# Kernel optimization log

Measured on AMD Instinct MI355X. Metric: run time of the kernel, lower is better.

Reference implementation:

```python
import jax, jax.numpy as jnp
import numpy as np

B, C = 2048, 5000          # batchSize, classNum
LLR_REL = 0.9              # keep-rate; k = ceil(B*C*(1-llr_rel))
K = int(np.ceil(B * C * (1.0 - LLR_REL)))
MARGIN = 0.0


def _bce_with_logits(x, t):
    # elementwise BCEWithLogitsLoss (reduce=False): max(x,0) - x*t + log1p(exp(-|x|))
    return jnp.maximum(x, 0.0) - x * t + jnp.log1p(jnp.exp(-jnp.abs(x)))


def setup_inputs() -> dict:
    key = jax.random.key(0)
    k1, k2 = jax.random.split(key)
    inp = jax.random.normal(k1, (B, C), dtype=jnp.float32)
    # target in {-1, 0, +1}: -1 negative, 0 unobserved/ignored, +1 positive
    tgt = (jax.random.randint(k2, (B, C), 0, 3) - 1).astype(jnp.float32)
    return {"input": inp, "target": tgt, "k": K}


def reference(input, target, k):
    input = input.astype(jnp.float32)
    target = target.astype(jnp.float32)
    positive_mask = (target > MARGIN).astype(jnp.float32)
    negative_mask = (target < -MARGIN).astype(jnp.float32)
    positive_loss = _bce_with_logits(input, target)
    negative_loss = _bce_with_logits(-input, -target)
    unobserved_loss = negative_mask * negative_loss
    if k != 0:
        # k-th largest value of the flattened unobserved loss is the threshold
        topk_vals = jax.lax.top_k(unobserved_loss.reshape(-1), k)[0]
        topk_lossvalue = topk_vals[-1]
        loss_mask = (unobserved_loss < topk_lossvalue).astype(jnp.float32)
        negative_mask = negative_mask * loss_mask
    loss = positive_mask * positive_loss + negative_mask * negative_loss
    return loss
```

## Files before the change

kernel.cpp:

```cpp
#include <hip/hip_runtime.h>
#include <cstdint>


struct SelState {
    uint32_t prefix;
    uint32_t k_rem;
    uint32_t u_kth;
    float    thr_nl;
    uint32_t done;
};

#define GUARD 256u

__device__ __forceinline__ uint32_t xform(uint32_t b) {
    return ((int32_t)b < 0) ? ~b : (b | 0x80000000u);
}
__device__ __forceinline__ float unxform(uint32_t u) {
    uint32_t b = (u & 0x80000000u) ? (u ^ 0x80000000u) : ~u;
    return __uint_as_float(b);
}
__device__ __forceinline__ float neg_loss_precise(float x, float t) {
#pragma clang fp contract(off)
    return (fmaxf(-x, 0.0f) - x * t) + log1pf(expf(-fabsf(x)));
}

__device__ __forceinline__ void hist_quad(uint32_t* my, float4 xv, float4 tv) {
    uint32_t u0 = (tv.x < 0.0f) ? xform(__float_as_uint(xv.x)) : 0u;
    uint32_t u1 = (tv.y < 0.0f) ? xform(__float_as_uint(xv.y)) : 0u;
    uint32_t u2 = (tv.z < 0.0f) ? xform(__float_as_uint(xv.z)) : 0u;
    uint32_t u3 = (tv.w < 0.0f) ? xform(__float_as_uint(xv.w)) : 0u;
    if (u0) atomicAdd(&my[u0 >> 21], 1u);
    if (u1) atomicAdd(&my[u1 >> 21], 1u);
    if (u2) atomicAdd(&my[u2 >> 21], 1u);
    if (u3) atomicAdd(&my[u3 >> 21], 1u);
}

__global__ __launch_bounds__(256) void k1_hist(
        const float* __restrict__ x, const float* __restrict__ t,
        uint32_t* __restrict__ hist, int n) {
    __shared__ uint32_t lh[2 * 2049];
    for (int i = threadIdx.x; i < 2 * 2049; i += 256) lh[i] = 0;
    __syncthreads();
    uint32_t* my = &lh[(threadIdx.x & 1) * 2049];

    const float4* x4 = (const float4*)x;
    const float4* t4 = (const float4*)t;
    const int n4 = n >> 2;
    const int S = gridDim.x * 256;
    int i = blockIdx.x * 256 + threadIdx.x;
    for (; i + 3 * S < n4; i += 4 * S) {
        float4 xa = x4[i], xb = x4[i + S], xc = x4[i + 2 * S], xd = x4[i + 3 * S];
        float4 ta = t4[i], tb = t4[i + S], tc = t4[i + 2 * S], td = t4[i + 3 * S];
        hist_quad(my, xa, ta);
        hist_quad(my, xb, tb);
        hist_quad(my, xc, tc);
        hist_quad(my, xd, td);
    }
    for (; i < n4; i += S) {
        float4 xa = x4[i], ta = t4[i];
        hist_quad(my, xa, ta);
    }
    if (blockIdx.x == 0) {
        for (int j = (n4 << 2) + threadIdx.x; j < n; j += 256) {
            uint32_t u = (t[j] < 0.0f) ? xform(__float_as_uint(x[j])) : 0u;
            if (u) atomicAdd(&my[u >> 21], 1u);
        }
    }
    __syncthreads();
    for (int b = threadIdx.x; b < 2048; b += 256) {
        uint32_t c = lh[b] + lh[2049 + b];
        if (c) atomicAdd(&hist[b], c);
    }
}

__global__ __launch_bounds__(256) void scan1(
        const uint32_t* __restrict__ hist, SelState* __restrict__ st,
        const int* __restrict__ kptr) {
    __shared__ uint32_t part[256];
    const int tid = threadIdx.x;
    uint32_t cnt[8];
    uint32_t lsum = 0;
#pragma unroll
    for (int j = 0; j < 8; ++j) { cnt[j] = hist[tid * 8 + j]; lsum += cnt[j]; }
    part[tid] = lsum;
    __syncthreads();
    for (int off = 1; off < 256; off <<= 1) {
        uint32_t add = (tid + off < 256) ? part[tid + off] : 0u;
        __syncthreads();
        part[tid] += add;
        __syncthreads();
    }
    const uint32_t total = part[0];
    int kk = *kptr;
    uint32_t k = (kk > 0) ? (uint32_t)kk : 0u;
    if (k == 0u) {
        if (tid == 0) { st->u_kth = 0xFFFFFFFFu; st->thr_nl = __int_as_float(0x7F800000); st->done = 1u; }
        return;
    }
    if (k > total) {
        if (tid == 0) { st->u_kth = 0u; st->thr_nl = 0.0f; st->done = 1u; }
        return;
    }
    uint32_t A = (tid < 255) ? part[tid + 1] : 0u;
#pragma unroll
    for (int j = 7; j >= 0; --j) {
        uint32_t c = cnt[j];
        if (A < k && k <= A + c) {
            st->prefix = (uint32_t)(tid * 8 + j);
            st->k_rem = k - A;
        }
        A += c;
    }
}

__device__ __forceinline__ void cnt_quad(uint32_t* __restrict__ h21, uint32_t pref,
                                         float4 xv, float4 tv) {
    uint32_t u0 = (tv.x < 0.0f) ? xform(__float_as_uint(xv.x)) : 0u;
    uint32_t u1 = (tv.y < 0.0f) ? xform(__float_as_uint(xv.y)) : 0u;
    uint32_t u2 = (tv.z < 0.0f) ? xform(__float_as_uint(xv.z)) : 0u;
    uint32_t u3 = (tv.w < 0.0f) ? xform(__float_as_uint(xv.w)) : 0u;
    if (u0 && (u0 >> 21) == pref) atomicAdd(&h21[u0 & 0x1FFFFFu], 1u);
    if (u1 && (u1 >> 21) == pref) atomicAdd(&h21[u1 & 0x1FFFFFu], 1u);
    if (u2 && (u2 >> 21) == pref) atomicAdd(&h21[u2 & 0x1FFFFFu], 1u);
    if (u3 && (u3 >> 21) == pref) atomicAdd(&h21[u3 & 0x1FFFFFu], 1u);
}

__global__ __launch_bounds__(256) void k2_hist21(
        const float* __restrict__ x, const float* __restrict__ t,
        uint32_t* __restrict__ h21, const SelState* __restrict__ st, int n) {
    __shared__ uint32_t s_pref, s_done;
    if (threadIdx.x == 0) { s_pref = st->prefix; s_done = st->done; }
    __syncthreads();
    if (s_done) return;
    const uint32_t pref = s_pref;

    const float4* x4 = (const float4*)x;
    const float4* t4 = (const float4*)t;
    const int n4 = n >> 2;
    const int S = gridDim.x * 256;
    int i = blockIdx.x * 256 + threadIdx.x;
    for (; i + 3 * S < n4; i += 4 * S) {
        float4 xa = x4[i], xb = x4[i + S], xc = x4[i + 2 * S], xd = x4[i + 3 * S];
        float4 ta = t4[i], tb = t4[i + S], tc = t4[i + 2 * S], td = t4[i + 3 * S];
        cnt_quad(h21, pref, xa, ta);
        cnt_quad(h21, pref, xb, tb);
        cnt_quad(h21, pref, xc, tc);
        cnt_quad(h21, pref, xd, td);
    }
    for (; i < n4; i += S) {
        float4 xa = x4[i], ta = t4[i];
        cnt_quad(h21, pref, xa, ta);
    }
    if (blockIdx.x == 0) {
        for (int j = (n4 << 2) + threadIdx.x; j < n; j += 256) {
            uint32_t u = (t[j] < 0.0f) ? xform(__float_as_uint(x[j])) : 0u;
            if (u && (u >> 21) == pref) atomicAdd(&h21[u & 0x1FFFFFu], 1u);
        }
    }
}

__global__ __launch_bounds__(256) void scan2a(
        const uint32_t* __restrict__ h21, uint32_t* __restrict__ csums,
        const SelState* __restrict__ st) {
    __shared__ uint32_t red[256];
    __shared__ uint32_t s_done;
    if (threadIdx.x == 0) s_done = st->done;
    __syncthreads();
    if (s_done) return;
    const uint4* b4 = (const uint4*)(h21 + (size_t)blockIdx.x * 2048);
    uint32_t s = 0;
    for (int j = threadIdx.x; j < 512; j += 256) {
        uint4 v = b4[j];
        s += v.x + v.y + v.z + v.w;
    }
    red[threadIdx.x] = s;
    __syncthreads();
    for (int off = 128; off > 0; off >>= 1) {
        if (threadIdx.x < off) red[threadIdx.x] += red[threadIdx.x + off];
        __syncthreads();
    }
    if (threadIdx.x == 0) csums[blockIdx.x] = red[0];
}

__global__ __launch_bounds__(256) void scan2b(
        const uint32_t* __restrict__ h21, const uint32_t* __restrict__ csums,
        SelState* __restrict__ st) {
    __shared__ uint32_t part[256];
    __shared__ uint32_t sel[2];
    __shared__ SelState sst;
    const int tid = threadIdx.x;
    if (tid == 0) sst = *st;
    __syncthreads();
    if (sst.done) return;
    const uint32_t k = sst.k_rem;

    uint32_t c4[4];
    uint32_t lsum = 0;
#pragma unroll
    for (int j = 0; j < 4; ++j) { c4[j] = csums[tid * 4 + j]; lsum += c4[j]; }
    part[tid] = lsum;
    __syncthreads();
    for (int off = 1; off < 256; off <<= 1) {
        uint32_t add = (tid + off < 256) ? part[tid + off] : 0u;
        __syncthreads();
        part[tid] += add;
        __syncthreads();
    }
    uint32_t A = (tid < 255) ? part[tid + 1] : 0u;
#pragma unroll
    for (int j = 3; j >= 0; --j) {
        uint32_t c = c4[j];
        if (A < k && k <= A + c) { sel[0] = (uint32_t)(tid * 4 + j); sel[1] = k - A; }
        A += c;
    }
    __syncthreads();
    const uint32_t chunk = sel[0];
    const uint32_t k2 = sel[1];
    __syncthreads();

    const uint32_t* base = h21 + (size_t)chunk * 2048;
    uint32_t b8[8];
    lsum = 0;
#pragma unroll
    for (int j = 0; j < 8; ++j) { b8[j] = base[tid * 8 + j]; lsum += b8[j]; }
    part[tid] = lsum;
    __syncthreads();
    for (int off = 1; off < 256; off <<= 1) {
        uint32_t add = (tid + off < 256) ? part[tid + off] : 0u;
        __syncthreads();
        part[tid] += add;
        __syncthreads();
    }
    A = (tid < 255) ? part[tid + 1] : 0u;
#pragma unroll
    for (int j = 7; j >= 0; --j) {
        uint32_t c = b8[j];
        if (A < k2 && k2 <= A + c) {
            uint32_t u = (sst.prefix << 21) | (chunk * 2048u + (uint32_t)(tid * 8 + j));
            st->u_kth = u;
            st->thr_nl = neg_loss_precise(unxform(u), -1.0f);
            st->done = 1u;
        }
        A += c;
    }
}

__device__ __forceinline__ float fin1(float xx, float tt, uint32_t ukth, float thr) {
    float lp = __logf(1.0f + __expf(-fabsf(xx)));
    float v = 0.0f;
    if (tt > 0.0f) {
        v = fmaxf(xx, 0.0f) - xx * tt + lp;
    } else if (tt < 0.0f) {
        uint32_t u = xform(__float_as_uint(xx));
        bool keep = u < ukth;
        if (keep && (ukth - u) < GUARD)
            keep = neg_loss_precise(xx, tt) < thr;
        if (keep) v = fmaxf(-xx, 0.0f) - xx * tt + lp;
    }
    return v;
}

__device__ __forceinline__ float4 fin_quad(float4 xv, float4 tv, uint32_t ukth, float thr) {
    float4 r;
    r.x = fin1(xv.x, tv.x, ukth, thr);
    r.y = fin1(xv.y, tv.y, ukth, thr);
    r.z = fin1(xv.z, tv.z, ukth, thr);
    r.w = fin1(xv.w, tv.w, ukth, thr);
    return r;
}

__global__ __launch_bounds__(256) void k_final(
        const float* __restrict__ x, const float* __restrict__ t,
        const SelState* __restrict__ st, float* __restrict__ out, int n) {
    const uint32_t ukth = st->u_kth;
    const float thr = st->thr_nl;
    const float4* x4 = (const float4*)x;
    const float4* t4 = (const float4*)t;
    float4* o4 = (float4*)out;
    const int n4 = n >> 2;
    const int S = gridDim.x * 256;
    int i = blockIdx.x * 256 + threadIdx.x;
    for (; i + 3 * S < n4; i += 4 * S) {
        float4 xa = x4[i], xb = x4[i + S], xc = x4[i + 2 * S], xd = x4[i + 3 * S];
        float4 ta = t4[i], tb = t4[i + S], tc = t4[i + 2 * S], td = t4[i + 3 * S];
        o4[i]         = fin_quad(xa, ta, ukth, thr);
        o4[i + S]     = fin_quad(xb, tb, ukth, thr);
        o4[i + 2 * S] = fin_quad(xc, tc, ukth, thr);
        o4[i + 3 * S] = fin_quad(xd, td, ukth, thr);
    }
    for (; i < n4; i += S) {
        float4 xa = x4[i], ta = t4[i];
        o4[i] = fin_quad(xa, ta, ukth, thr);
    }
    if (blockIdx.x == 0) {
        for (int j = (n4 << 2) + threadIdx.x; j < n; j += 256) {
            out[j] = fin1(x[j], t[j], ukth, thr);
        }
    }
}

extern "C" void kernel_launch(void* const* d_in, const int* in_sizes, int n_in,
                              void* d_out, int out_size, void* d_ws, size_t ws_size,
                              hipStream_t stream) {
    const float* x = (const float*)d_in[0];
    const float* t = (const float*)d_in[1];
    const int* kptr = (const int*)d_in[2];
    float* out = (float*)d_out;
    const int n = in_sizes[0];
    if (n <= 0) return;

    char* ws = (char*)d_ws;
    uint32_t* hist1 = (uint32_t*)(ws + 0);
    uint32_t* csums = (uint32_t*)(ws + 8192);
    SelState* st    = (SelState*)(ws + 12288);
    uint32_t* h21   = (uint32_t*)(ws + 16384);

    hipMemsetAsync(d_ws, 0, 16384 + (size_t)(1u << 21) * 4u, stream);

    const int n4 = n >> 2;
    int work = (n4 + 255) / 256;
    if (work < 1) work = 1;
    int grid = work < 1024 ? work : 1024;

    k1_hist  <<<grid, 256, 0, stream>>>(x, t, hist1, n);
    scan1    <<<1, 256, 0, stream>>>(hist1, st, kptr);
    k2_hist21<<<grid, 256, 0, stream>>>(x, t, h21, st, n);
    scan2a   <<<1024, 256, 0, stream>>>(h21, csums, st);
    scan2b   <<<1, 256, 0, stream>>>(h21, csums, st);
    k_final  <<<grid, 256, 0, stream>>>(x, t, st, out, n);
}
```

Before: 177.1 us.

## Compact negative candidates in first pass and refine radix select on compacted list

The first histogram pass now also stream-compacts the transformed keys of negative-target elements into per-wave segments and stores a packed 2-bit class map for each float4 of targets. The second and third radix refinement passes read only the compacted candidates instead of re-reading both full input arrays, and the 8 MB second-level histogram memset is replaced by two small histograms (10-bit and 11-bit). The final pass reads the byte class map instead of the float target array. This cuts global memory traffic and the large memset, at the cost of one extra small kernel and extra writes of candidates and cmap in the first pass.

```diff
diff --git a/kernel.cpp b/kernel.cpp
--- a/kernel.cpp
+++ b/kernel.cpp
@@ -1,10 +1,13 @@
 #include <hip/hip_runtime.h>
 #include <cstdint>
+#include <cstddef>
 
 
 struct SelState {
-    uint32_t prefix;
-    uint32_t k_rem;
+    uint32_t prefix1;
+    uint32_t k1rem;
+    uint32_t prefix2;
+    uint32_t k2rem;
     uint32_t u_kth;
     float    thr_nl;
     uint32_t done;
@@ -24,22 +27,41 @@
     return (fmaxf(-x, 0.0f) - x * t) + log1pf(expf(-fabsf(x)));
 }
 
-__device__ __forceinline__ void hist_quad(uint32_t* my, float4 xv, float4 tv) {
-    uint32_t u0 = (tv.x < 0.0f) ? xform(__float_as_uint(xv.x)) : 0u;
-    uint32_t u1 = (tv.y < 0.0f) ? xform(__float_as_uint(xv.y)) : 0u;
-    uint32_t u2 = (tv.z < 0.0f) ? xform(__float_as_uint(xv.z)) : 0u;
-    uint32_t u3 = (tv.w < 0.0f) ? xform(__float_as_uint(xv.w)) : 0u;
+__device__ __forceinline__ void wscan(uint32_t m, int lane, uint32_t& excl, uint32_t& tot) {
+    uint32_t inc = m;
+#pragma unroll
+    for (int d = 1; d < 64; d <<= 1) {
+        uint32_t v = __shfl_up(inc, (unsigned)d, 64);
+        if (lane >= d) inc += v;
+    }
+    excl = inc - m;
+    tot = __shfl(inc, 63, 64);
+}
+
+__device__ __forceinline__ uint32_t quad_u_cls(uint32_t* my, float4 xv, float4 tv,
+        uint32_t& u0, uint32_t& u1, uint32_t& u2, uint32_t& u3) {
+    u0 = (tv.x < 0.0f) ? xform(__float_as_uint(xv.x)) : 0u;
+    u1 = (tv.y < 0.0f) ? xform(__float_as_uint(xv.y)) : 0u;
+    u2 = (tv.z < 0.0f) ? xform(__float_as_uint(xv.z)) : 0u;
+    u3 = (tv.w < 0.0f) ? xform(__float_as_uint(xv.w)) : 0u;
+    uint32_t cls = ((tv.x > 0.0f) ? 1u : ((tv.x < 0.0f) ? 2u : 0u))
+                 | (((tv.y > 0.0f) ? 1u : ((tv.y < 0.0f) ? 2u : 0u)) << 2)
+                 | (((tv.z > 0.0f) ? 1u : ((tv.z < 0.0f) ? 2u : 0u)) << 4)
+                 | (((tv.w > 0.0f) ? 1u : ((tv.w < 0.0f) ? 2u : 0u)) << 6);
     if (u0) atomicAdd(&my[u0 >> 21], 1u);
     if (u1) atomicAdd(&my[u1 >> 21], 1u);
     if (u2) atomicAdd(&my[u2 >> 21], 1u);
     if (u3) atomicAdd(&my[u3 >> 21], 1u);
+    return cls;
 }
 
 __global__ __launch_bounds__(256) void k1_hist(
         const float* __restrict__ x, const float* __restrict__ t,
-        uint32_t* __restrict__ hist, int n) {
+        uint32_t* __restrict__ hist1, uint32_t* __restrict__ cand1,
+        uint32_t* __restrict__ wvcnt, uint8_t* __restrict__ cmap,
+        int n, int segw) {
     __shared__ uint32_t lh[2 * 2049];
-    for (int i = threadIdx.x; i < 2 * 2049; i += 256) lh[i] = 0;
+    for (int j = threadIdx.x; j < 2 * 2049; j += 256) lh[j] = 0;
     __syncthreads();
     uint32_t* my = &lh[(threadIdx.x & 1) * 2049];
 
@@ -47,41 +69,108 @@
     const float4* t4 = (const float4*)t;
     const int n4 = n >> 2;
     const int S = gridDim.x * 256;
+    const int lane = threadIdx.x & 63;
+    const int wid  = threadIdx.x >> 6;
+    uint32_t* wseg = cand1 + (size_t)(blockIdx.x * 4 + wid) * (size_t)segw;
+    uint32_t wcur = 0;
+
+    int M4 = 0;
+    {
+        long rem = (long)n4 - 1 - (long)(blockIdx.x * 256 + 255);
+        if (rem >= 0) {
+            long T = rem / S;
+            if (T >= 3) M4 = (int)((T - 3) / 4 + 1);
+        }
+    }
     int i = blockIdx.x * 256 + threadIdx.x;
-    for (; i + 3 * S < n4; i += 4 * S) {
+
+    for (int b = 0; b < M4; ++b, i += 4 * S) {
         float4 xa = x4[i], xb = x4[i + S], xc = x4[i + 2 * S], xd = x4[i + 3 * S];
         float4 ta = t4[i], tb = t4[i + S], tc = t4[i + 2 * S], td = t4[i + 3 * S];
-        hist_quad(my, xa, ta);
-        hist_quad(my, xb, tb);
-        hist_quad(my, xc, tc);
-        hist_quad(my, xd, td);
-    }
-    for (; i < n4; i += S) {
-        float4 xa = x4[i], ta = t4[i];
-        hist_quad(my, xa, ta);
-    }
+        uint32_t u0, u1, u2, u3, u4_, u5, u6, u7, u8, u9, uA, uB, uC, uD, uE, uF;
+        uint32_t ca = quad_u_cls(my, xa, ta, u0, u1, u2, u3);
+        uint32_t cb = quad_u_cls(my, xb, tb, u4_, u5, u6, u7);
+        uint32_t cc = quad_u_cls(my, xc, tc, u8, u9, uA, uB);
+        uint32_t cd = quad_u_cls(my, xd, td, uC, uD, uE, uF);
+        cmap[i]         = (uint8_t)ca;
+        cmap[i + S]     = (uint8_t)cb;
+        cmap[i + 2 * S] = (uint8_t)cc;
+        cmap[i + 3 * S] = (uint8_t)cd;
+        uint32_t m = (u0 != 0) + (u1 != 0) + (u2 != 0) + (u3 != 0)
+                   + (u4_ != 0) + (u5 != 0) + (u6 != 0) + (u7 != 0)
+                   + (u8 != 0) + (u9 != 0) + (uA != 0) + (uB != 0)
+                   + (uC != 0) + (uD != 0) + (uE != 0) + (uF != 0);
+        uint32_t excl, tot;
+        wscan(m, lane, excl, tot);
+        uint32_t p = wcur + excl;
+        if (u0)  wseg[p++] = u0;
+        if (u1)  wseg[p++] = u1;
+        if (u2)  wseg[p++] = u2;
+        if (u3)  wseg[p++] = u3;
+        if (u4_) wseg[p++] = u4_;
+        if (u5)  wseg[p++] = u5;
+        if (u6)  wseg[p++] = u6;
+        if (u7)  wseg[p++] = u7;
+        if (u8)  wseg[p++] = u8;
+        if (u9)  wseg[p++] = u9;
+        if (uA)  wseg[p++] = uA;
+        if (uB)  wseg[p++] = uB;
+        if (uC)  wseg[p++] = uC;
+        if (uD)  wseg[p++] = uD;
+        if (uE)  wseg[p++] = uE;
+        if (uF)  wseg[p++] = uF;
+        wcur += tot;
+    }
+
+    for (; __any(i < n4); i += S) {
+        const bool act = i < n4;
+        float4 xa = act ? x4[i] : make_float4(0.f, 0.f, 0.f, 0.f);
+        float4 ta = act ? t4[i] : make_float4(0.f, 0.f, 0.f, 0.f);
+        uint32_t u0, u1, u2, u3;
+        uint32_t ca = quad_u_cls(my, xa, ta, u0, u1, u2, u3);
+        if (act) cmap[i] = (uint8_t)ca;
+        uint32_t m = (u0 != 0) + (u1 != 0) + (u2 != 0) + (u3 != 0);
+        uint32_t excl, tot;
+        wscan(m, lane, excl, tot);
+        uint32_t p = wcur + excl;
+        if (u0) wseg[p++] = u0;
+        if (u1) wseg[p++] = u1;
+        if (u2) wseg[p++] = u2;
+        if (u3) wseg[p++] = u3;
+        wcur += tot;
+    }
+
     if (blockIdx.x == 0) {
-        for (int j = (n4 << 2) + threadIdx.x; j < n; j += 256) {
-            uint32_t u = (t[j] < 0.0f) ? xform(__float_as_uint(x[j])) : 0u;
-            if (u) atomicAdd(&my[u >> 21], 1u);
-        }
-    }
-    __syncthreads();
-    for (int b = threadIdx.x; b < 2048; b += 256) {
-        uint32_t c = lh[b] + lh[2049 + b];
-        if (c) atomicAdd(&hist[b], c);
-    }
-}
-
-__global__ __launch_bounds__(256) void scan1(
-        const uint32_t* __restrict__ hist, SelState* __restrict__ st,
+        int j = (n4 << 2) + threadIdx.x;
+        const bool act = j < n;
+        float xx = act ? x[j] : 0.0f;
+        float tt = act ? t[j] : 0.0f;
+        uint32_t u0 = (tt < 0.0f) ? xform(__float_as_uint(xx)) : 0u;
+        if (u0) atomicAdd(&my[u0 >> 21], 1u);
+        uint32_t excl, tot;
+        wscan(u0 != 0 ? 1u : 0u, lane, excl, tot);
+        if (u0) wseg[wcur + excl] = u0;
+        wcur += tot;
+    }
+
+    if (lane == 0) wvcnt[blockIdx.x * 4 + wid] = wcur;
+
+    __syncthreads();
+    for (int b2 = threadIdx.x; b2 < 2048; b2 += 256) {
+        uint32_t c = lh[b2] + lh[2049 + b2];
+        if (c) atomicAdd(&hist1[b2], c);
+    }
+}
+
+__global__ __launch_bounds__(256) void s1_scan(
+        const uint32_t* __restrict__ hist1, SelState* __restrict__ st,
         const int* __restrict__ kptr) {
     __shared__ uint32_t part[256];
     const int tid = threadIdx.x;
     uint32_t cnt[8];
     uint32_t lsum = 0;
 #pragma unroll
-    for (int j = 0; j < 8; ++j) { cnt[j] = hist[tid * 8 + j]; lsum += cnt[j]; }
+    for (int j = 0; j < 8; ++j) { cnt[j] = hist1[tid * 8 + j]; lsum += cnt[j]; }
     part[tid] = lsum;
     __syncthreads();
     for (int off = 1; off < 256; off <<= 1) {
@@ -106,98 +195,50 @@
     for (int j = 7; j >= 0; --j) {
         uint32_t c = cnt[j];
         if (A < k && k <= A + c) {
-            st->prefix = (uint32_t)(tid * 8 + j);
-            st->k_rem = k - A;
+            st->prefix1 = (uint32_t)(tid * 8 + j);
+            st->k1rem = k - A;
         }
         A += c;
     }
 }
 
-__device__ __forceinline__ void cnt_quad(uint32_t* __restrict__ h21, uint32_t pref,
-                                         float4 xv, float4 tv) {
-    uint32_t u0 = (tv.x < 0.0f) ? xform(__float_as_uint(xv.x)) : 0u;
-    uint32_t u1 = (tv.y < 0.0f) ? xform(__float_as_uint(xv.y)) : 0u;
-    uint32_t u2 = (tv.z < 0.0f) ? xform(__float_as_uint(xv.z)) : 0u;
-    uint32_t u3 = (tv.w < 0.0f) ? xform(__float_as_uint(xv.w)) : 0u;
-    if (u0 && (u0 >> 21) == pref) atomicAdd(&h21[u0 & 0x1FFFFFu], 1u);
-    if (u1 && (u1 >> 21) == pref) atomicAdd(&h21[u1 & 0x1FFFFFu], 1u);
-    if (u2 && (u2 >> 21) == pref) atomicAdd(&h21[u2 & 0x1FFFFFu], 1u);
-    if (u3 && (u3 >> 21) == pref) atomicAdd(&h21[u3 & 0x1FFFFFu], 1u);
-}
-
-__global__ __launch_bounds__(256) void k2_hist21(
-        const float* __restrict__ x, const float* __restrict__ t,
-        uint32_t* __restrict__ h21, const SelState* __restrict__ st, int n) {
+__global__ __launch_bounds__(256) void k2_hist2(
+        const uint32_t* __restrict__ cand1, const uint32_t* __restrict__ wvcnt,
+        uint32_t* __restrict__ hist2, const SelState* __restrict__ st,
+        int nseg, int segw) {
     __shared__ uint32_t s_pref, s_done;
-    if (threadIdx.x == 0) { s_pref = st->prefix; s_done = st->done; }
+    if (threadIdx.x == 0) { s_pref = st->prefix1; s_done = st->done; }
     __syncthreads();
     if (s_done) return;
     const uint32_t pref = s_pref;
-
-    const float4* x4 = (const float4*)x;
-    const float4* t4 = (const float4*)t;
-    const int n4 = n >> 2;
-    const int S = gridDim.x * 256;
-    int i = blockIdx.x * 256 + threadIdx.x;
-    for (; i + 3 * S < n4; i += 4 * S) {
-        float4 xa = x4[i], xb = x4[i + S], xc = x4[i + 2 * S], xd = x4[i + 3 * S];
-        float4 ta = t4[i], tb = t4[i + S], tc = t4[i + 2 * S], td = t4[i + 3 * S];
-        cnt_quad(h21, pref, xa, ta);
-        cnt_quad(h21, pref, xb, tb);
-        cnt_quad(h21, pref, xc, tc);
-        cnt_quad(h21, pref, xd, td);
-    }
-    for (; i < n4; i += S) {
-        float4 xa = x4[i], ta = t4[i];
-        cnt_quad(h21, pref, xa, ta);
-    }
-    if (blockIdx.x == 0) {
-        for (int j = (n4 << 2) + threadIdx.x; j < n; j += 256) {
-            uint32_t u = (t[j] < 0.0f) ? xform(__float_as_uint(x[j])) : 0u;
-            if (u && (u >> 21) == pref) atomicAdd(&h21[u & 0x1FFFFFu], 1u);
-        }
-    }
-}
-
-__global__ __launch_bounds__(256) void scan2a(
-        const uint32_t* __restrict__ h21, uint32_t* __restrict__ csums,
-        const SelState* __restrict__ st) {
-    __shared__ uint32_t red[256];
-    __shared__ uint32_t s_done;
-    if (threadIdx.x == 0) s_done = st->done;
-    __syncthreads();
-    if (s_done) return;
-    const uint4* b4 = (const uint4*)(h21 + (size_t)blockIdx.x * 2048);
-    uint32_t s = 0;
-    for (int j = threadIdx.x; j < 512; j += 256) {
-        uint4 v = b4[j];
-        s += v.x + v.y + v.z + v.w;
-    }
-    red[threadIdx.x] = s;
-    __syncthreads();
-    for (int off = 128; off > 0; off >>= 1) {
-        if (threadIdx.x < off) red[threadIdx.x] += red[threadIdx.x + off];
-        __syncthreads();
-    }
-    if (threadIdx.x == 0) csums[blockIdx.x] = red[0];
-}
-
-__global__ __launch_bounds__(256) void scan2b(
-        const uint32_t* __restrict__ h21, const uint32_t* __restrict__ csums,
-        SelState* __restrict__ st) {
+    for (int s = blockIdx.x; s < nseg; s += gridDim.x) {
+        const uint32_t cnt = wvcnt[s];
+        const uint32_t* base = cand1 + (size_t)s * (size_t)segw;
+        const uint4* b4 = (const uint4*)base;
+        const uint32_t c4 = cnt >> 2;
+        for (uint32_t j = threadIdx.x; j < c4; j += 256) {
+            uint4 v = b4[j];
+            if ((v.x >> 21) == pref) atomicAdd(&hist2[(v.x >> 11) & 1023u], 1u);
+            if ((v.y >> 21) == pref) atomicAdd(&hist2[(v.y >> 11) & 1023u], 1u);
+            if ((v.z >> 21) == pref) atomicAdd(&hist2[(v.z >> 11) & 1023u], 1u);
+            if ((v.w >> 21) == pref) atomicAdd(&hist2[(v.w >> 11) & 1023u], 1u);
+        }
+        if (threadIdx.x < (cnt & 3u)) {
+            uint32_t u = base[(c4 << 2) + threadIdx.x];
+            if ((u >> 21) == pref) atomicAdd(&hist2[(u >> 11) & 1023u], 1u);
+        }
+    }
+}
+
+__global__ __launch_bounds__(256) void s2_scan(
+        const uint32_t* __restrict__ hist2, SelState* __restrict__ st) {
+    if (st->done) return;
     __shared__ uint32_t part[256];
-    __shared__ uint32_t sel[2];
-    __shared__ SelState sst;
     const int tid = threadIdx.x;
-    if (tid == 0) sst = *st;
-    __syncthreads();
-    if (sst.done) return;
-    const uint32_t k = sst.k_rem;
-
-    uint32_t c4[4];
+    uint32_t cnt[4];
     uint32_t lsum = 0;
 #pragma unroll
-    for (int j = 0; j < 4; ++j) { c4[j] = csums[tid * 4 + j]; lsum += c4[j]; }
+    for (int j = 0; j < 4; ++j) { cnt[j] = hist2[tid * 4 + j]; lsum += cnt[j]; }
     part[tid] = lsum;
     __syncthreads();
     for (int off = 1; off < 256; off <<= 1) {
@@ -206,23 +247,59 @@
         part[tid] += add;
         __syncthreads();
     }
+    const uint32_t k = st->k1rem;
     uint32_t A = (tid < 255) ? part[tid + 1] : 0u;
 #pragma unroll
     for (int j = 3; j >= 0; --j) {
-        uint32_t c = c4[j];
-        if (A < k && k <= A + c) { sel[0] = (uint32_t)(tid * 4 + j); sel[1] = k - A; }
+        uint32_t c = cnt[j];
+        if (A < k && k <= A + c) {
+            st->prefix2 = (uint32_t)(tid * 4 + j);
+            st->k2rem = k - A;
+        }
         A += c;
     }
-    __syncthreads();
-    const uint32_t chunk = sel[0];
-    const uint32_t k2 = sel[1];
-    __syncthreads();
-
-    const uint32_t* base = h21 + (size_t)chunk * 2048;
-    uint32_t b8[8];
-    lsum = 0;
-#pragma unroll
-    for (int j = 0; j < 8; ++j) { b8[j] = base[tid * 8 + j]; lsum += b8[j]; }
+}
+
+__global__ __launch_bounds__(256) void k3_hist3(
+        const uint32_t* __restrict__ cand1, const uint32_t* __restrict__ wvcnt,
+        uint32_t* __restrict__ hist3, const SelState* __restrict__ st,
+        int nseg, int segw) {
+    __shared__ uint32_t s_pref21, s_done;
+    if (threadIdx.x == 0) {
+        s_pref21 = (st->prefix1 << 10) | st->prefix2;
+        s_done = st->done;
+    }
+    __syncthreads();
+    if (s_done) return;
+    const uint32_t pref21 = s_pref21;
+    for (int s = blockIdx.x; s < nseg; s += gridDim.x) {
+        const uint32_t cnt = wvcnt[s];
+        const uint32_t* base = cand1 + (size_t)s * (size_t)segw;
+        const uint4* b4 = (const uint4*)base;
+        const uint32_t c4 = cnt >> 2;
+        for (uint32_t j = threadIdx.x; j < c4; j += 256) {
+            uint4 v = b4[j];
+            if ((v.x >> 11) == pref21) atomicAdd(&hist3[v.x & 0x7FFu], 1u);
+            if ((v.y >> 11) == pref21) atomicAdd(&hist3[v.y & 0x7FFu], 1u);
+            if ((v.z >> 11) == pref21) atomicAdd(&hist3[v.z & 0x7FFu], 1u);
+            if ((v.w >> 11) == pref21) atomicAdd(&hist3[v.w & 0x7FFu], 1u);
+        }
+        if (threadIdx.x < (cnt & 3u)) {
+            uint32_t u = base[(c4 << 2) + threadIdx.x];
+            if ((u >> 11) == pref21) atomicAdd(&hist3[u & 0x7FFu], 1u);
+        }
+    }
+}
+
+__global__ __launch_bounds__(256) void s3_scan(
+        const uint32_t* __restrict__ hist3, SelState* __restrict__ st) {
+    if (st->done) return;
+    __shared__ uint32_t part[256];
+    const int tid = threadIdx.x;
+    uint32_t cnt[8];
+    uint32_t lsum = 0;
+#pragma unroll
+    for (int j = 0; j < 8; ++j) { cnt[j] = hist3[tid * 8 + j]; lsum += cnt[j]; }
     part[tid] = lsum;
     __syncthreads();
     for (int off = 1; off < 256; off <<= 1) {
@@ -231,12 +308,13 @@
         part[tid] += add;
         __syncthreads();
     }
-    A = (tid < 255) ? part[tid + 1] : 0u;
+    const uint32_t k = st->k2rem;
+    uint32_t A = (tid < 255) ? part[tid + 1] : 0u;
 #pragma unroll
     for (int j = 7; j >= 0; --j) {
-        uint32_t c = b8[j];
-        if (A < k2 && k2 <= A + c) {
-            uint32_t u = (sst.prefix << 21) | (chunk * 2048u + (uint32_t)(tid * 8 + j));
+        uint32_t c = cnt[j];
+        if (A < k && k <= A + c) {
+            uint32_t u = (st->prefix1 << 21) | (st->prefix2 << 11) | (uint32_t)(tid * 8 + j);
             st->u_kth = u;
             st->thr_nl = neg_loss_precise(unxform(u), -1.0f);
             st->done = 1u;
@@ -245,7 +323,31 @@
     }
 }
 
-__device__ __forceinline__ float fin1(float xx, float tt, uint32_t ukth, float thr) {
+__device__ __forceinline__ float fin1c(float xx, uint32_t cls, uint32_t ukth, float thr) {
+    float lp = __logf(1.0f + __expf(-fabsf(xx)));
+    float v = 0.0f;
+    if (cls == 1u) {
+        v = (fmaxf(xx, 0.0f) - xx) + lp;
+    } else if (cls == 2u) {
+        uint32_t u = xform(__float_as_uint(xx));
+        bool keep = u < ukth;
+        if (keep && (ukth - u) < GUARD)
+            keep = neg_loss_precise(xx, -1.0f) < thr;
+        if (keep) v = (fmaxf(-xx, 0.0f) + xx) + lp;
+    }
+    return v;
+}
+
+__device__ __forceinline__ float4 fin_quadc(float4 xv, uint32_t cb, uint32_t ukth, float thr) {
+    float4 r;
+    r.x = fin1c(xv.x, cb & 3u, ukth, thr);
+    r.y = fin1c(xv.y, (cb >> 2) & 3u, ukth, thr);
+    r.z = fin1c(xv.z, (cb >> 4) & 3u, ukth, thr);
+    r.w = fin1c(xv.w, (cb >> 6) & 3u, ukth, thr);
+    return r;
+}
+
+__device__ __forceinline__ float fin1t(float xx, float tt, uint32_t ukth, float thr) {
     float lp = __logf(1.0f + __expf(-fabsf(xx)));
     float v = 0.0f;
     if (tt > 0.0f) {
@@ -260,41 +362,33 @@
     return v;
 }
 
-__device__ __forceinline__ float4 fin_quad(float4 xv, float4 tv, uint32_t ukth, float thr) {
-    float4 r;
-    r.x = fin1(xv.x, tv.x, ukth, thr);
-    r.y = fin1(xv.y, tv.y, ukth, thr);
-    r.z = fin1(xv.z, tv.z, ukth, thr);
-    r.w = fin1(xv.w, tv.w, ukth, thr);
-    return r;
-}
-
 __global__ __launch_bounds__(256) void k_final(
         const float* __restrict__ x, const float* __restrict__ t,
-        const SelState* __restrict__ st, float* __restrict__ out, int n) {
+        const uint8_t* __restrict__ cmap, const SelState* __restrict__ st,
+        float* __restrict__ out, int n) {
     const uint32_t ukth = st->u_kth;
     const float thr = st->thr_nl;
     const float4* x4 = (const float4*)x;
-    const float4* t4 = (const float4*)t;
     float4* o4 = (float4*)out;
     const int n4 = n >> 2;
     const int S = gridDim.x * 256;
     int i = blockIdx.x * 256 + threadIdx.x;
     for (; i + 3 * S < n4; i += 4 * S) {
         float4 xa = x4[i], xb = x4[i + S], xc = x4[i + 2 * S], xd = x4[i + 3 * S];
-        float4 ta = t4[i], tb = t4[i + S], tc = t4[i + 2 * S], td = t4[i + 3 * S];
-        o4[i]         = fin_quad(xa, ta, ukth, thr);
-        o4[i + S]     = fin_quad(xb, tb, ukth, thr);
-        o4[i + 2 * S] = fin_quad(xc, tc, ukth, thr);
-        o4[i + 3 * S] = fin_quad(xd, td, ukth, thr);
+        uint32_t ca = cmap[i], cb = cmap[i + S], cc = cmap[i + 2 * S], cd = cmap[i + 3 * S];
+        o4[i]         = fin_quadc(xa, ca, ukth, thr);
+        o4[i + S]     = fin_quadc(xb, cb, ukth, thr);
+        o4[i + 2 * S] = fin_quadc(xc, cc, ukth, thr);
+        o4[i + 3 * S] = fin_quadc(xd, cd, ukth, thr);
     }
     for (; i < n4; i += S) {
-        float4 xa = x4[i], ta = t4[i];
-        o4[i] = fin_quad(xa, ta, ukth, thr);
+        float4 xa = x4[i];
+        uint32_t ca = cmap[i];
+        o4[i] = fin_quadc(xa, ca, ukth, thr);
     }
     if (blockIdx.x == 0) {
         for (int j = (n4 << 2) + threadIdx.x; j < n; j += 256) {
-            out[j] = fin1(x[j], t[j], ukth, thr);
+            out[j] = fin1t(x[j], t[j], ukth, thr);
         }
     }
 }
@@ -309,23 +403,32 @@
     const int n = in_sizes[0];
     if (n <= 0) return;
 
-    char* ws = (char*)d_ws;
-    uint32_t* hist1 = (uint32_t*)(ws + 0);
-    uint32_t* csums = (uint32_t*)(ws + 8192);
-    SelState* st    = (SelState*)(ws + 12288);
-    uint32_t* h21   = (uint32_t*)(ws + 16384);
-
-    hipMemsetAsync(d_ws, 0, 16384 + (size_t)(1u << 21) * 4u, stream);
-
     const int n4 = n >> 2;
     int work = (n4 + 255) / 256;
     if (work < 1) work = 1;
     int grid = work < 1024 ? work : 1024;
-
-    k1_hist  <<<grid, 256, 0, stream>>>(x, t, hist1, n);
-    scan1    <<<1, 256, 0, stream>>>(hist1, st, kptr);
-    k2_hist21<<<grid, 256, 0, stream>>>(x, t, h21, st, n);
-    scan2a   <<<1024, 256, 0, stream>>>(h21, csums, st);
-    scan2b   <<<1, 256, 0, stream>>>(h21, csums, st);
-    k_final  <<<grid, 256, 0, stream>>>(x, t, st, out, n);
-}
+    const int S = grid * 256;
+    const int Q = (n4 + S - 1) / S;
+    const int segw = 256 * Q + 4;
+    const int nseg = grid * 4;
+
+    char* ws = (char*)d_ws;
+    uint32_t* hist1 = (uint32_t*)(ws + 0);
+    uint32_t* hist2 = (uint32_t*)(ws + 8192);
+    uint32_t* hist3 = (uint32_t*)(ws + 12288);
+    SelState* st    = (SelState*)(ws + 20480);
+    uint32_t* wvcnt = (uint32_t*)(ws + 24576);
+    uint8_t*  cmap  = (uint8_t*)(ws + 40960);
+    size_t c1off = (40960 + (size_t)n4 + 255) & ~(size_t)255;
+    uint32_t* cand1 = (uint32_t*)(ws + c1off);
+
+    hipMemsetAsync(d_ws, 0, 20544, stream);
+
+    k1_hist <<<grid, 256, 0, stream>>>(x, t, hist1, cand1, wvcnt, cmap, n, segw);
+    s1_scan <<<1, 256, 0, stream>>>(hist1, st, kptr);
+    k2_hist2<<<grid, 256, 0, stream>>>(cand1, wvcnt, hist2, st, nseg, segw);
+    s2_scan <<<1, 256, 0, stream>>>(hist2, st);
+    k3_hist3<<<grid, 256, 0, stream>>>(cand1, wvcnt, hist3, st, nseg, segw);
+    s3_scan <<<1, 256, 0, stream>>>(hist3, st);
+    k_final <<<grid, 256, 0, stream>>>(x, t, cmap, st, out, n);
+}
```

New measurement: 207.9 us. +17.4%, slower.
